# Kernel tuning notes

Measured on AMD Instinct MI355X. Metric: run time of the kernel, lower is better.

Reference implementation:

```python
import jax, jax.numpy as jnp
import numpy as np

B, C_IN, H, W_IN = 32, 128, 64, 64
C_OUT, K = 256, 3


def setup_inputs() -> dict:
    key = jax.random.key(0)
    kx, kw = jax.random.split(key)
    x = jax.random.normal(kx, (B, C_IN, H, W_IN), dtype=jnp.float32)
    # original initializes weights as binary {0,1} floats
    W = jax.random.randint(kw, (C_OUT, C_IN, K, K), 0, 2).astype(jnp.float32)
    return {"x": x, "W": W}


def reference(x, W):
    # XOR-style conv: out[b,co,ho,wo] = sum(patch * (1 - 2*W[co]))
    # stride=1, padding=0 (hardcoded in the original forward).
    eff_w = 1.0 - 2.0 * W  # (C_OUT, C_IN, K, K)
    return jax.lax.conv_general_dilated(
        x, eff_w,
        window_strides=(1, 1),
        padding='VALID',
        dimension_numbers=('NCHW', 'OIHW', 'NCHW'),
    )
```

## Files before the change

### kernel.cpp

```cpp
#include <hip/hip_runtime.h>


typedef __bf16 bf16x8 __attribute__((ext_vector_type(8)));
typedef float  f32x4  __attribute__((ext_vector_type(4)));

#define CIPAD 40

__global__ void prepack_w_kernel(const float* __restrict__ Wf,
                                 unsigned short* __restrict__ effw) {
  int idx = blockIdx.x * 256 + threadIdx.x;
  if (idx >= 9 * 4 * 16 * 64 * 8) return;
  int j    = idx & 7;
  int lane = (idx >> 3) & 63;
  int tile = (idx >> 9) & 15;
  int cc   = (idx >> 13) & 3;
  int e    = idx >> 15;
  int co = tile * 16 + (lane & 15);
  int ci = cc * 32 + (lane >> 4) * 8 + j;
  float w = Wf[(co * 128 + ci) * 9 + e];
  __bf16 h = (__bf16)(1.0f - 2.0f * w);
  unsigned short u; __builtin_memcpy(&u, &h, 2);
  effw[idx] = u;
}

__global__ __launch_bounds__(256, 2)
void xorconv_mfma_kernel(const float* __restrict__ x,
                         const unsigned short* __restrict__ effw,
                         float* __restrict__ out) {
  __shared__ __align__(16) unsigned short xs[6 * 66 * CIPAD];

  const int tid    = threadIdx.x;
  const int bxc    = blockIdx.x;
  const int co_blk = bxc * 128;
  const int hbase  = blockIdx.y * 4;
  const int bb     = blockIdx.z;

  const int wv   = tid >> 6;
  const int lane = tid & 63;
  const int quad = lane >> 4;
  const int l16  = lane & 15;

  f32x4 acc[8][4];
  #pragma unroll
  for (int i = 0; i < 8; ++i)
    #pragma unroll
    for (int j = 0; j < 4; ++j)
      acc[i][j] = (f32x4){0.f, 0.f, 0.f, 0.f};

  unsigned int* xs32 = (unsigned int*)xs;

  for (int cc = 0; cc < 4; ++cc) {
    const int c0 = cc * 32;

    for (int p2 = tid; p2 < 6 * 33 * 16; p2 += 256) {
      int c2  = p2 % 33;
      int t2  = p2 / 33;
      int ci2 = t2 & 15;
      int r   = t2 >> 4;
      int c   = c2 * 2;
      int h_in = hbase + r; if (h_in > 63) h_in = 63;
      int c_in = c;         if (c_in > 62) c_in = 62;
      const float* gp = x + (((size_t)(bb * 128 + c0 + ci2 * 2) * 64 + h_in) * 64 + c_in);
      float f00 = gp[0],    f01 = gp[1];
      float f10 = gp[4096], f11 = gp[4097];
      __bf16 h00 = (__bf16)f00, h01 = (__bf16)f01, h10 = (__bf16)f10, h11 = (__bf16)f11;
      unsigned short u00, u01, u10, u11;
      __builtin_memcpy(&u00, &h00, 2); __builtin_memcpy(&u01, &h01, 2);
      __builtin_memcpy(&u10, &h10, 2); __builtin_memcpy(&u11, &h11, 2);
      xs32[(r * 66 + c) * (CIPAD / 2) + ci2]     = (unsigned)u00 | ((unsigned)u10 << 16);
      xs32[(r * 66 + c + 1) * (CIPAD / 2) + ci2] = (unsigned)u01 | ((unsigned)u11 << 16);
    }
    __syncthreads();

    for (int e = 0; e < 9; ++e) {
      const int kh = e / 3;
      const int kw = e - 3 * kh;
      const int rr = wv + kh;

      bf16x8 bfr[4];
      #pragma unroll
      for (int j = 0; j < 4; ++j) {
        int ccol = j * 16 + l16 + kw;
        bfr[j] = *(const bf16x8*)&xs[(rr * 66 + ccol) * CIPAD + quad * 8];
      }
      const unsigned short* wp =
          effw + ((((size_t)e * 4 + cc) * 16 + bxc * 8) * 64 + lane) * 8;
      #pragma unroll
      for (int mt = 0; mt < 8; ++mt) {
        bf16x8 af = *(const bf16x8*)(wp + (size_t)mt * 512);
        #pragma unroll
        for (int j = 0; j < 4; ++j)
          acc[mt][j] = __builtin_amdgcn_mfma_f32_16x16x32_bf16(af, bfr[j], acc[mt][j], 0, 0, 0);
      }
    }
    __syncthreads();
  }

  const int ho = hbase + wv;
  if (ho < 62) {
    #pragma unroll
    for (int mt = 0; mt < 8; ++mt) {
      const int co = co_blk + mt * 16 + quad * 4;
      #pragma unroll
      for (int j = 0; j < 4; ++j) {
        const int wo = j * 16 + l16;
        if (wo < 62) {
          float* op = out + (((size_t)(bb * 256 + co) * 62 + ho) * 62 + wo);
          #pragma unroll
          for (int rg = 0; rg < 4; ++rg)
            op[(size_t)rg * 3844] = acc[mt][j][rg];
        }
      }
    }
  }
}

extern "C" void kernel_launch(void* const* d_in, const int* in_sizes, int n_in,
                              void* d_out, int out_size, void* d_ws, size_t ws_size,
                              hipStream_t stream) {
  const float* x  = (const float*)d_in[0];
  const float* Wf = (const float*)d_in[1];
  float* out = (float*)d_out;
  unsigned short* effw = (unsigned short*)d_ws;

  prepack_w_kernel<<<dim3((9 * 4 * 16 * 64 * 8 + 255) / 256), dim3(256), 0, stream>>>(Wf, effw);

  dim3 grid(2, 16, 32);
  xorconv_mfma_kernel<<<grid, dim3(256), 0, stream>>>(x, effw, out);
}
```

Before: 285.0 us.

## Retile conv to 64 channels by 8 rows per block with prefetched weights

Each block now covers 64 output channels and 8 output rows instead of 128 channels and 4 rows. Each wave computes two rows, so every weight fragment is reused across twice as many MFMAs, and the input halo overhead per row drops. Weight fragments are double-buffered in registers and the next tap is prefetched while the current one is computed, with the prepacked layout reordered so successive taps are contiguous. Input staging now loads four channels per thread and writes 8-byte stores. Shared memory grows to 10 rows and the channel tile is halved, so input tiles are loaded twice as often across the grid. Register pressure also rises.

```diff
diff --git a/kernel.cpp b/kernel.cpp
--- a/kernel.cpp
+++ b/kernel.cpp
@@ -9,12 +9,13 @@
 __global__ void prepack_w_kernel(const float* __restrict__ Wf,
                                  unsigned short* __restrict__ effw) {
   int idx = blockIdx.x * 256 + threadIdx.x;
-  if (idx >= 9 * 4 * 16 * 64 * 8) return;
+  if (idx >= 36 * 16 * 64 * 8) return;
   int j    = idx & 7;
   int lane = (idx >> 3) & 63;
   int tile = (idx >> 9) & 15;
-  int cc   = (idx >> 13) & 3;
-  int e    = idx >> 15;
+  int g    = idx >> 13;
+  int e    = g % 9;
+  int cc   = g / 9;
   int co = tile * 16 + (lane & 15);
   int ci = cc * 32 + (lane >> 4) * 8 + j;
   float w = Wf[(co * 128 + ci) * 9 + e];
@@ -23,16 +24,24 @@
   effw[idx] = u;
 }
 
+__device__ __forceinline__ unsigned int pack_bf16(float a, float b) {
+  __bf16 ha = (__bf16)a, hb = (__bf16)b;
+  unsigned short ua, ub;
+  __builtin_memcpy(&ua, &ha, 2);
+  __builtin_memcpy(&ub, &hb, 2);
+  return (unsigned)ua | ((unsigned)ub << 16);
+}
+
 __global__ __launch_bounds__(256, 2)
 void xorconv_mfma_kernel(const float* __restrict__ x,
                          const unsigned short* __restrict__ effw,
                          float* __restrict__ out) {
-  __shared__ __align__(16) unsigned short xs[6 * 66 * CIPAD];
+  __shared__ __align__(16) unsigned short xs[10 * 66 * CIPAD];
 
   const int tid    = threadIdx.x;
   const int bxc    = blockIdx.x;
-  const int co_blk = bxc * 128;
-  const int hbase  = blockIdx.y * 4;
+  const int co_blk = bxc * 64;
+  const int hbase  = blockIdx.y * 8;
   const int bb     = blockIdx.z;
 
   const int wv   = tid >> 6;
@@ -40,75 +49,99 @@
   const int quad = lane >> 4;
   const int l16  = lane & 15;
 
-  f32x4 acc[8][4];
+  f32x4 acc[2][4][4];
   #pragma unroll
-  for (int i = 0; i < 8; ++i)
+  for (int rw = 0; rw < 2; ++rw)
     #pragma unroll
-    for (int j = 0; j < 4; ++j)
-      acc[i][j] = (f32x4){0.f, 0.f, 0.f, 0.f};
+    for (int i = 0; i < 4; ++i)
+      #pragma unroll
+      for (int j = 0; j < 4; ++j)
+        acc[rw][i][j] = (f32x4){0.f, 0.f, 0.f, 0.f};
 
   unsigned int* xs32 = (unsigned int*)xs;
+
+  const unsigned short* wbase = effw + ((size_t)(bxc * 4) * 64 + lane) * 8;
+  bf16x8 afb[2][4];
+  #pragma unroll
+  for (int mt = 0; mt < 4; ++mt)
+    afb[0][mt] = *(const bf16x8*)(wbase + mt * 512);
 
   for (int cc = 0; cc < 4; ++cc) {
     const int c0 = cc * 32;
 
-    for (int p2 = tid; p2 < 6 * 33 * 16; p2 += 256) {
-      int c2  = p2 % 33;
-      int t2  = p2 / 33;
-      int ci2 = t2 & 15;
-      int r   = t2 >> 4;
-      int c   = c2 * 2;
+    for (int p = tid; p < 10 * 33 * 8; p += 256) {
+      int c2 = p % 33;
+      int t  = p / 33;
+      int cp = t & 7;
+      int r  = t >> 3;
+      int c  = c2 * 2;
       int h_in = hbase + r; if (h_in > 63) h_in = 63;
       int c_in = c;         if (c_in > 62) c_in = 62;
-      const float* gp = x + (((size_t)(bb * 128 + c0 + ci2 * 2) * 64 + h_in) * 64 + c_in);
-      float f00 = gp[0],    f01 = gp[1];
-      float f10 = gp[4096], f11 = gp[4097];
-      __bf16 h00 = (__bf16)f00, h01 = (__bf16)f01, h10 = (__bf16)f10, h11 = (__bf16)f11;
-      unsigned short u00, u01, u10, u11;
-      __builtin_memcpy(&u00, &h00, 2); __builtin_memcpy(&u01, &h01, 2);
-      __builtin_memcpy(&u10, &h10, 2); __builtin_memcpy(&u11, &h11, 2);
-      xs32[(r * 66 + c) * (CIPAD / 2) + ci2]     = (unsigned)u00 | ((unsigned)u10 << 16);
-      xs32[(r * 66 + c + 1) * (CIPAD / 2) + ci2] = (unsigned)u01 | ((unsigned)u11 << 16);
+      const float* gp = x + ((size_t)(bb * 128 + c0 + cp * 4) * 4096 + h_in * 64 + c_in);
+      float a0 = gp[0],     a1 = gp[1];
+      float b0 = gp[4096],  b1 = gp[4097];
+      float e0 = gp[8192],  e1 = gp[8193];
+      float g0 = gp[12288], g1 = gp[12289];
+      uint2 w0 = {pack_bf16(a0, b0), pack_bf16(e0, g0)};
+      uint2 w1 = {pack_bf16(a1, b1), pack_bf16(e1, g1)};
+      *(uint2*)&xs32[(r * 66 + c)     * (CIPAD / 2) + cp * 2] = w0;
+      *(uint2*)&xs32[(r * 66 + c + 1) * (CIPAD / 2) + cp * 2] = w1;
     }
     __syncthreads();
 
+    #pragma unroll
     for (int e = 0; e < 9; ++e) {
-      const int kh = e / 3;
-      const int kw = e - 3 * kh;
-      const int rr = wv + kh;
+      const int cur = e & 1, nxt = cur ^ 1;
+      const int kh = e / 3, kw = e % 3;
 
-      bf16x8 bfr[4];
+      {
+        int lin  = cc * 9 + e;
+        int linn = lin < 35 ? lin + 1 : 35;
+        const unsigned short* wp = wbase + (size_t)linn * 8192;
+        #pragma unroll
+        for (int mt = 0; mt < 4; ++mt)
+          afb[nxt][mt] = *(const bf16x8*)(wp + mt * 512);
+      }
+
       #pragma unroll
-      for (int j = 0; j < 4; ++j) {
-        int ccol = j * 16 + l16 + kw;
-        bfr[j] = *(const bf16x8*)&xs[(rr * 66 + ccol) * CIPAD + quad * 8];
-      }
-      const unsigned short* wp =
-          effw + ((((size_t)e * 4 + cc) * 16 + bxc * 8) * 64 + lane) * 8;
-      #pragma unroll
-      for (int mt = 0; mt < 8; ++mt) {
-        bf16x8 af = *(const bf16x8*)(wp + (size_t)mt * 512);
+      for (int rw = 0; rw < 2; ++rw) {
+        const int rr = wv * 2 + rw + kh;
+        bf16x8 bfr[4];
         #pragma unroll
-        for (int j = 0; j < 4; ++j)
-          acc[mt][j] = __builtin_amdgcn_mfma_f32_16x16x32_bf16(af, bfr[j], acc[mt][j], 0, 0, 0);
+        for (int j = 0; j < 4; ++j) {
+          int ccol = j * 16 + l16 + kw;
+          bfr[j] = *(const bf16x8*)&xs[(rr * 66 + ccol) * CIPAD + quad * 8];
+        }
+        #pragma unroll
+        for (int mt = 0; mt < 4; ++mt)
+          #pragma unroll
+          for (int j = 0; j < 4; ++j)
+            acc[rw][mt][j] = __builtin_amdgcn_mfma_f32_16x16x32_bf16(
+                afb[cur][mt], bfr[j], acc[rw][mt][j], 0, 0, 0);
       }
     }
     __syncthreads();
+
+    #pragma unroll
+    for (int mt = 0; mt < 4; ++mt) afb[0][mt] = afb[1][mt];
   }
 
-  const int ho = hbase + wv;
-  if (ho < 62) {
-    #pragma unroll
-    for (int mt = 0; mt < 8; ++mt) {
-      const int co = co_blk + mt * 16 + quad * 4;
+  #pragma unroll
+  for (int rw = 0; rw < 2; ++rw) {
+    const int ho = hbase + wv * 2 + rw;
+    if (ho < 62) {
       #pragma unroll
-      for (int j = 0; j < 4; ++j) {
-        const int wo = j * 16 + l16;
-        if (wo < 62) {
-          float* op = out + (((size_t)(bb * 256 + co) * 62 + ho) * 62 + wo);
-          #pragma unroll
-          for (int rg = 0; rg < 4; ++rg)
-            op[(size_t)rg * 3844] = acc[mt][j][rg];
+      for (int mt = 0; mt < 4; ++mt) {
+        const int co = co_blk + mt * 16 + quad * 4;
+        #pragma unroll
+        for (int j = 0; j < 4; ++j) {
+          const int wo = j * 16 + l16;
+          if (wo < 62) {
+            float* op = out + (((size_t)(bb * 256 + co) * 62 + ho) * 62 + wo);
+            #pragma unroll
+            for (int rg = 0; rg < 4; ++rg)
+              op[(size_t)rg * 3844] = acc[rw][mt][j][rg];
+          }
         }
       }
     }
@@ -123,8 +156,8 @@
   float* out = (float*)d_out;
   unsigned short* effw = (unsigned short*)d_ws;
 
-  prepack_w_kernel<<<dim3((9 * 4 * 16 * 64 * 8 + 255) / 256), dim3(256), 0, stream>>>(Wf, effw);
+  prepack_w_kernel<<<dim3((36 * 16 * 64 * 8 + 255) / 256), dim3(256), 0, stream>>>(Wf, effw);
 
-  dim3 grid(2, 16, 32);
+  dim3 grid(4, 8, 32);
   xorconv_mfma_kernel<<<grid, dim3(256), 0, stream>>>(x, effw, out);
 }
```

Result: faster. 269.7 us (-5.4%).
